# Optimization experiments

Hardware: AMD Instinct MI355X
Metric: run time of the kernel (lower is better)

The kernel has to match this reference:

```python
import jax, jax.numpy as jnp
import numpy as np

N_P, N_I, DIM = 30, 40, 6
W_I, C1, C2, LAM = 0.7, 1.5, 1.5, 0.3
EPS = 1e-8


def _decode(pos):
    # pos: [P, 6] -> per-particle fusion weights via pairwise softmax
    e = jnp.exp(pos[:, :4])
    fg_s = e[:, 0] + e[:, 1] + EPS
    bg_s = e[:, 2] + e[:, 3] + EPS
    return e[:, 0] / fg_s, e[:, 1] / fg_s, e[:, 2] / bg_s, e[:, 3] / bg_s


def _fitness(pos, rgb, dep, mask, r_dep):
    # rgb, dep, mask, r_dep: [H, W]; pos: [P, 6] -> scores [P]
    rgb_fg, dep_fg, rgb_bg, dep_bg = _decode(pos)
    mn = mask - mask.mean()
    mn_norm = jnp.linalg.norm(mn) + EPS
    fg = rgb_fg[:, None, None] * rgb + dep_fg[:, None, None] * dep   # [P,H,W]
    bg = rgb_bg[:, None, None] * rgb + dep_bg[:, None, None] * dep
    fused = mask * fg + (1.0 - mask) * bg
    fn = fused - fused.mean(axis=(1, 2), keepdims=True)
    fn_norm = jnp.sqrt((fn * fn).sum(axis=(1, 2)))
    ncc = (fn * mn).sum(axis=(1, 2)) / (fn_norm * mn_norm + EPS)
    pen_fg = ((1.0 - r_dep) * mask).mean()
    pen_bg = ((1.0 - r_dep) * (1.0 - mask)).mean()
    rel_pen = dep_fg * pen_fg + dep_bg * pen_bg
    return ncc - LAM * rel_pen


def _pso(rgb, dep, mask, r_dep):
    # Deterministic PSO with fixed RNG key; inputs are [H, W] maps.
    key = jax.random.key(42)
    k_pos, k_vel, k_r1, k_r2 = jax.random.split(key, 4)
    pos = jax.random.uniform(k_pos, (N_P, DIM), minval=-2.0, maxval=2.0)
    vel = jax.random.uniform(k_vel, (N_P, DIM), minval=-0.5, maxval=0.5)
    r1s = jax.random.uniform(k_r1, (N_I, N_P, DIM))
    r2s = jax.random.uniform(k_r2, (N_I, N_P, DIM))

    pb_pos = pos
    pb_fit = _fitness(pos, rgb, dep, mask, r_dep)
    gi = jnp.argmax(pb_fit)
    gb_pos = pb_pos[gi]
    gb_fit = pb_fit[gi]

    def step(carry, rs):
        pos, vel, pb_pos, pb_fit, gb_pos, gb_fit = carry
        r1, r2 = rs
        vel = W_I * vel + C1 * r1 * (pb_pos - pos) + C2 * r2 * (gb_pos - pos)
        pos = jnp.clip(pos + vel, -3.0, 3.0)
        fit = _fitness(pos, rgb, dep, mask, r_dep)
        better = fit > pb_fit
        pb_pos = jnp.where(better[:, None], pos, pb_pos)
        pb_fit = jnp.where(better, fit, pb_fit)
        bi = jnp.argmax(pb_fit)
        improve = pb_fit[bi] > gb_fit
        gb_pos = jnp.where(improve, pb_pos[bi], gb_pos)
        gb_fit = jnp.where(improve, pb_fit[bi], gb_fit)
        return (pos, vel, pb_pos, pb_fit, gb_pos, gb_fit), None

    (pos, vel, pb_pos, pb_fit, gb_pos, gb_fit), _ = jax.lax.scan(
        step, (pos, vel, pb_pos, pb_fit, gb_pos, gb_fit), (r1s, r2s))
    rgb_fg, dep_fg, rgb_bg, dep_bg = _decode(gb_pos[None, :])
    return rgb_fg[0], dep_fg[0], rgb_bg[0], dep_bg[0]


def _cos_sim(feat, proto):
    # feat [B,C,H,W], proto [B,C] -> [B,H,W]; matches F.normalize (clamp_min eps)
    p = proto / jnp.maximum(jnp.linalg.norm(proto, axis=1, keepdims=True), 1e-12)
    fnorm = jnp.maximum(jnp.sqrt((feat * feat).sum(axis=1, keepdims=True)), 1e-12)
    f = feat / fnorm
    return jnp.einsum('bchw,bc->bhw', f, p)


def setup_inputs() -> dict:
    key = jax.random.key(0)
    ks = jax.random.split(key, 10)
    B, C, H, W = 8, 256, 64, 64
    return {
        'f_rgb': jax.random.normal(ks[0], (B, C, H, W), dtype=jnp.float32),
        'f_depth': jax.random.normal(ks[1], (B, C, H, W), dtype=jnp.float32),
        'r_rgb': jax.random.uniform(ks[2], (B, 1, H, W), dtype=jnp.float32),
        'r_depth': jax.random.uniform(ks[3], (B, 1, H, W), dtype=jnp.float32),
        'proto_rgb': jax.random.normal(ks[4], (B, C), dtype=jnp.float32),
        'proto_dep': jax.random.normal(ks[5], (B, C), dtype=jnp.float32),
        'query_mask': jax.random.uniform(ks[6], (B, 1, H, W), dtype=jnp.float32),
        'conv_w': jax.random.normal(ks[7], (C, C), dtype=jnp.float32) * 0.05,
        'bn_gamma': jax.random.uniform(ks[8], (C,), dtype=jnp.float32),
        'bn_beta': jax.random.normal(ks[9], (C,), dtype=jnp.float32) * 0.1,
        'bn_mean': jnp.zeros((C,), dtype=jnp.float32),
        'bn_var': jnp.ones((C,), dtype=jnp.float32),
    }


def reference(f_rgb, f_depth, r_rgb, r_depth, proto_rgb, proto_dep, query_mask,
              conv_w, bn_gamma, bn_beta, bn_mean, bn_var):
    # cosine similarity maps [B,H,W]
    rgb_sim = _cos_sim(f_rgb, proto_rgb)
    dep_sim = _cos_sim(f_depth, proto_dep)

    # PSO operates on detached batch-mean maps (torch .detach().mean(0).cpu())
    sg = jax.lax.stop_gradient
    np_rgb = sg(rgb_sim).mean(axis=0)                 # [H,W]
    np_dep = sg(dep_sim).mean(axis=0)                 # [H,W]
    np_mask = sg(query_mask)[:, 0].mean(axis=0)       # mask already at (H,W): nearest interp is identity
    np_r_dep = sg(r_depth)[:, 0].mean(axis=0)
    rgb_fg, dep_fg, rgb_bg, dep_bg = _pso(np_rgb, np_dep, np_mask, np_r_dep)

    f_fg = rgb_fg * f_rgb + dep_fg * f_depth
    f_bg = rgb_bg * f_rgb + dep_bg * f_depth
    proxy = jax.nn.sigmoid((rgb_sim + dep_sim)[:, None] * 3.0)   # [B,1,H,W]
    f_fused = proxy * f_fg + (1.0 - proxy) * f_bg

    # post_proj: 1x1 conv (no bias) -> BN (eval) -> ReLU
    y = jnp.einsum('oc,bchw->bohw', conv_w, f_fused)
    inv = bn_gamma / jnp.sqrt(bn_var + 1e-5)
    y = y * inv[None, :, None, None] + (bn_beta - bn_mean * inv)[None, :, None, None]
    return jax.nn.relu(y)
```

## Files before the change

### kernel.cpp

```cpp
#include <hip/hip_runtime.h>
#include <stdint.h>
#include <float.h>

static constexpr size_t WS_SIM_RGB = 4096;
static constexpr size_t WS_SIM_DEP = 36864;
static constexpr size_t WS_NPMAPS  = 69632;
static constexpr size_t WS_STATS   = 86016;
static constexpr size_t WS_POUT    = 86048;
static constexpr size_t WS_RNG     = 90112;

typedef short short8 __attribute__((ext_vector_type(8)));
typedef float f32x4 __attribute__((ext_vector_type(4)));

__device__ __forceinline__ uint32_t pack_bf2(float a, float b) {
  uint32_t ua = __float_as_uint(a), ub = __float_as_uint(b);
  uint32_t ra = (ua + 0x7fffu + ((ua >> 16) & 1u)) >> 16;
  uint32_t rb = (ub + 0x7fffu + ((ub >> 16) & 1u)) >> 16;
  return (ra & 0xffffu) | (rb << 16);
}

__device__ __forceinline__ void threefry2x32(uint32_t k0, uint32_t k1,
                                             uint32_t c0, uint32_t c1,
                                             uint32_t& o0, uint32_t& o1) {
  uint32_t ks2 = k0 ^ k1 ^ 0x1BD11BDAu;
  uint32_t x0 = c0 + k0;
  uint32_t x1 = c1 + k1;
#define TF_ROUND(r) { x0 += x1; x1 = (x1 << (r)) | (x1 >> (32 - (r))); x1 ^= x0; }
  TF_ROUND(13) TF_ROUND(15) TF_ROUND(26) TF_ROUND(6)
  x0 += k1;  x1 += ks2 + 1u;
  TF_ROUND(17) TF_ROUND(29) TF_ROUND(16) TF_ROUND(24)
  x0 += ks2; x1 += k0 + 2u;
  TF_ROUND(13) TF_ROUND(15) TF_ROUND(26) TF_ROUND(6)
  x0 += k0;  x1 += k1 + 3u;
  TF_ROUND(17) TF_ROUND(29) TF_ROUND(16) TF_ROUND(24)
  x0 += k1;  x1 += ks2 + 4u;
  TF_ROUND(13) TF_ROUND(15) TF_ROUND(26) TF_ROUND(6)
  x0 += ks2; x1 += k0 + 5u;
#undef TF_ROUND
  o0 = x0; o1 = x1;
}

__device__ __forceinline__ float tf_u01(uint32_t k0, uint32_t k1, uint32_t idx) {
  uint32_t o0, o1;
  threefry2x32(k0, k1, 0u, idx, o0, o1);
  uint32_t bits = o0 ^ o1;
  uint32_t fb = (bits >> 9) | 0x3F800000u;
  return __uint_as_float(fb) - 1.0f;
}

__global__ __launch_bounds__(256) void sim_kernel(
    const float* __restrict__ f_rgb, const float* __restrict__ f_dep,
    const float* __restrict__ proto_rgb, const float* __restrict__ proto_dep,
    float* __restrict__ sim_rgb, float* __restrict__ sim_dep) {
  int tid = threadIdx.x;
  int bm = blockIdx.y;
  int b = bm >> 1, mo = bm & 1;
  const float* f  = mo ? f_dep : f_rgb;
  const float* pr = mo ? proto_dep : proto_rgb;
  float* sim = mo ? sim_dep : sim_rgb;
  __shared__ float shp[256];
  __shared__ float wsum[4];
  float pv = pr[b * 256 + tid];
  float ss0 = pv * pv;
#pragma unroll
  for (int off = 32; off > 0; off >>= 1) ss0 += __shfl_xor(ss0, off, 64);
  if ((tid & 63) == 0) wsum[tid >> 6] = ss0;
  __syncthreads();
  float nrm = fmaxf(sqrtf(wsum[0] + wsum[1] + wsum[2] + wsum[3]), 1e-12f);
  shp[tid] = pv / nrm;
  __syncthreads();
  int p = blockIdx.x * 256 + tid;
  const float* base = f + (size_t)b * 256 * 4096 + p;
  float dot = 0.f, ss = 0.f;
#pragma unroll 8
  for (int c = 0; c < 256; ++c) {
    float x = base[(size_t)c * 4096];
    dot += x * shp[c];
    ss  += x * x;
  }
  float fn = fmaxf(sqrtf(ss), 1e-12f);
  sim[b * 4096 + p] = dot / fn;
}

__global__ __launch_bounds__(256) void npmaps_kernel(
    const float* __restrict__ sim_rgb, const float* __restrict__ sim_dep,
    const float* __restrict__ qmask, const float* __restrict__ r_dep,
    float* __restrict__ npm) {
  int i = blockIdx.x * 256 + threadIdx.x;
  float sr = 0.f, sd = 0.f, sm = 0.f, sq = 0.f;
#pragma unroll
  for (int b = 0; b < 8; ++b) {
    sr += sim_rgb[b * 4096 + i];
    sd += sim_dep[b * 4096 + i];
    sm += qmask[b * 4096 + i];
    sq += r_dep[b * 4096 + i];
  }
  npm[i]          = sr * 0.125f;
  npm[4096 + i]   = sd * 0.125f;
  npm[8192 + i]   = sm * 0.125f;
  npm[12288 + i]  = sq * 0.125f;
}

__global__ __launch_bounds__(256) void stats_kernel(const float* __restrict__ npm,
                                                    float* __restrict__ stats) {
  const float* np_rgb  = npm;
  const float* np_dep  = npm + 4096;
  const float* np_mask = npm + 8192;
  const float* np_rdep = npm + 12288;
  __shared__ float col[17][257];
  __shared__ float res1[17];
  __shared__ float res2[5];
  int tid = threadIdx.x;
  float acc[17];
#pragma unroll
  for (int k = 0; k < 17; ++k) acc[k] = 0.f;
  for (int i = tid; i < 4096; i += 256) {
    float m = np_mask[i], r = np_rgb[i], d = np_dep[i], q = np_rdep[i];
    float om = 1.f - m;
    float M1 = m * r, M2 = m * d, M3 = om * r, M4 = om * d;
    acc[0] += m;
    acc[1] += M1; acc[2] += M2; acc[3] += M3; acc[4] += M4;
    acc[5] += M1 * M1; acc[6] += M1 * M2; acc[7] += M1 * M3; acc[8] += M1 * M4;
    acc[9] += M2 * M2; acc[10] += M2 * M3; acc[11] += M2 * M4;
    acc[12] += M3 * M3; acc[13] += M3 * M4; acc[14] += M4 * M4;
    float oq = 1.f - q;
    acc[15] += oq * m; acc[16] += oq * om;
  }
#pragma unroll
  for (int k = 0; k < 17; ++k) col[k][tid] = acc[k];
  __syncthreads();
  if (tid < 17) { float s = 0.f; for (int i = 0; i < 256; ++i) s += col[tid][i]; res1[tid] = s; }
  __syncthreads();
  float mask_mean = res1[0] * (1.f / 4096.f);
  float a2[5] = {0.f, 0.f, 0.f, 0.f, 0.f};
  for (int i = tid; i < 4096; i += 256) {
    float m = np_mask[i], r = np_rgb[i], d = np_dep[i];
    float om = 1.f - m;
    float mn = m - mask_mean;
    a2[0] += m * r * mn; a2[1] += m * d * mn;
    a2[2] += om * r * mn; a2[3] += om * d * mn;
    a2[4] += mn * mn;
  }
  __syncthreads();
#pragma unroll
  for (int k = 0; k < 5; ++k) col[k][tid] = a2[k];
  __syncthreads();
  if (tid < 5) { float s = 0.f; for (int i = 0; i < 256; ++i) s += col[tid][i]; res2[tid] = s; }
  __syncthreads();
  if (tid == 0) {
    stats[0] = res1[1]; stats[1] = res1[2]; stats[2] = res1[3]; stats[3] = res1[4];
    float G11 = res1[5], G12 = res1[6], G13 = res1[7], G14 = res1[8];
    float G22 = res1[9], G23 = res1[10], G24 = res1[11];
    float G33 = res1[12], G34 = res1[13], G44 = res1[14];
    float Gf[16] = {G11, G12, G13, G14,  G12, G22, G23, G24,
                    G13, G23, G33, G34,  G14, G24, G34, G44};
    for (int k = 0; k < 16; ++k) stats[4 + k] = Gf[k];
    stats[20] = res2[0]; stats[21] = res2[1]; stats[22] = res2[2]; stats[23] = res2[3];
    stats[24] = sqrtf(res2[4]) + 1e-8f;
    stats[25] = res1[15] * (1.f / 4096.f);
    stats[26] = res1[16] * (1.f / 4096.f);
  }
}

__global__ __launch_bounds__(256) void rng_kernel(float* __restrict__ rng) {
  int g = blockIdx.x * 256 + threadIdx.x;
  if (g >= 14760) return;
  int kind; uint32_t splitIdx, ctr, dst;
  if (g < 180) {
    kind = 0; splitIdx = 0; ctr = (uint32_t)g; dst = (uint32_t)g;
  } else if (g < 360) {
    kind = 1; splitIdx = 1; ctr = (uint32_t)(g - 180); dst = (uint32_t)g;
  } else if (g < 7560) {
    uint32_t c = (uint32_t)(g - 360);
    kind = 2; splitIdx = 2; ctr = c;
    uint32_t t = c / 180u, rem = c % 180u, p = rem / 6u, d = rem % 6u;
    dst = 360u + t * 360u + p * 12u + d;
  } else {
    uint32_t c = (uint32_t)(g - 7560);
    kind = 3; splitIdx = 3; ctr = c;
    uint32_t t = c / 180u, rem = c % 180u, p = rem / 6u, d = rem % 6u;
    dst = 360u + t * 360u + p * 12u + 6u + d;
  }
  uint32_t k0, k1;
  threefry2x32(0u, 42u, 0u, splitIdx, k0, k1);
  float u = tf_u01(k0, k1, ctr);
  float v;
  if (kind == 0)      v = fmaxf(-2.0f, u * 4.0f - 2.0f);
  else if (kind == 1) v = fmaxf(-0.5f, u - 0.5f);
  else                v = u;
  rng[dst] = v;
}

__device__ __forceinline__ float pso_fitness_fast(const float pos[6],
    const float S[4], const float G[16], const float V[4],
    float mn_norm, float pen_fg, float pen_bg) {
  float e0 = __expf(pos[0]), e1 = __expf(pos[1]);
  float e2 = __expf(pos[2]), e3 = __expf(pos[3]);
  float rf = __builtin_amdgcn_rcpf(e0 + e1 + 1e-8f);
  float rb = __builtin_amdgcn_rcpf(e2 + e3 + 1e-8f);
  float w[4] = {e0 * rf, e1 * rf, e2 * rb, e3 * rb};
  float num = 0.f, mus = 0.f;
#pragma unroll
  for (int k = 0; k < 4; ++k) { num += w[k] * V[k]; mus += w[k] * S[k]; }
  float q = 0.f;
#pragma unroll
  for (int j = 0; j < 4; ++j)
#pragma unroll
    for (int k = 0; k < 4; ++k) q += w[j] * G[j * 4 + k] * w[k];
  float fn2 = fmaxf(q - mus * mus * (1.f / 4096.f), 0.f);
  float den = __builtin_amdgcn_sqrtf(fn2) * mn_norm + 1e-8f;
  float ncc = num * __builtin_amdgcn_rcpf(den);
  return ncc - 0.3f * (w[1] * pen_fg + w[3] * pen_bg);
}

__device__ __forceinline__ float wavemax_lo32(float v) {
  int x = __float_as_int(v);
#define DPP_STEP(ctrl) { \
    int y = __builtin_amdgcn_update_dpp(x, x, ctrl, 0xf, 0xf, false); \
    x = __float_as_int(fmaxf(__int_as_float(x), __int_as_float(y))); }
  DPP_STEP(0x128)
  DPP_STEP(0x124)
  DPP_STEP(0x122)
  DPP_STEP(0x121)
#undef DPP_STEP
  float r0 = __int_as_float(__builtin_amdgcn_readlane(x, 0));
  float r1 = __int_as_float(__builtin_amdgcn_readlane(x, 16));
  return fmaxf(r0, r1);
}

__global__ void pso_kernel(const float* __restrict__ stats,
                           const float* __restrict__ rng,
                           float* __restrict__ pout) {
  int lane = threadIdx.x;
  bool act = lane < 30;
  float S[4], G[16], V[4];
#pragma unroll
  for (int k = 0; k < 4; ++k) S[k] = stats[k];
#pragma unroll
  for (int k = 0; k < 16; ++k) G[k] = stats[4 + k];
#pragma unroll
  for (int k = 0; k < 4; ++k) V[k] = stats[20 + k];
  float mn_norm = stats[24], pen_fg = stats[25], pen_bg = stats[26];

  float pos[6], vel[6], pbp[6];
#pragma unroll
  for (int d = 0; d < 6; ++d) { pos[d] = 0.f; vel[d] = 0.f; }
  if (act) {
#pragma unroll
    for (int d = 0; d < 6; ++d) {
      pos[d] = rng[lane * 6 + d];
      vel[d] = rng[180 + lane * 6 + d];
    }
  }
#pragma unroll
  for (int d = 0; d < 6; ++d) pbp[d] = pos[d];

  float f0 = pso_fitness_fast(pos, S, G, V, mn_norm, pen_fg, pen_bg);
  float pbf = act ? f0 : -FLT_MAX;

  float gbf = wavemax_lo32(pbf);
  float gb[6];
  {
    unsigned long long mm = __ballot(pbf == gbf);
    int bl = __ffsll(mm) - 1;
#pragma unroll
    for (int d = 0; d < 6; ++d)
      gb[d] = __int_as_float(__builtin_amdgcn_readlane(__float_as_int(pbp[d]), bl));
  }

  const float* rbase = rng + 360;
  float4 A0, A1, A2, B0, B1, B2;
  {
    const float4* p0 = (const float4*)(rbase + lane * 12);
    A0 = p0[0]; A1 = p0[1]; A2 = p0[2];
    const float4* p1 = (const float4*)(rbase + 360 + lane * 12);
    B0 = p1[0]; B1 = p1[1]; B2 = p1[2];
  }

#define PSO_ITER(R0, R1, R2, TNEXT) { \
    float r1v[6] = {R0.x, R0.y, R0.z, R0.w, R1.x, R1.y}; \
    float r2v[6] = {R1.z, R1.w, R2.x, R2.y, R2.z, R2.w}; \
    const float4* pf = (const float4*)(rbase + (TNEXT) * 360 + lane * 12); \
    R0 = pf[0]; R1 = pf[1]; R2 = pf[2]; \
    _Pragma("unroll") \
    for (int d = 0; d < 6; ++d) { \
      vel[d] = 0.7f * vel[d] + 1.5f * r1v[d] * (pbp[d] - pos[d]) \
                             + 1.5f * r2v[d] * (gb[d] - pos[d]); \
      pos[d] = fmaxf(-3.0f, fminf(pos[d] + vel[d], 3.0f)); \
    } \
    float f = pso_fitness_fast(pos, S, G, V, mn_norm, pen_fg, pen_bg); \
    if (act && f > pbf) { \
      pbf = f; \
      _Pragma("unroll") for (int d = 0; d < 6; ++d) pbp[d] = pos[d]; \
    } \
    float maxv = wavemax_lo32(pbf); \
    if (maxv > gbf) {     \
      unsigned long long mm = __ballot(pbf == maxv); \
      int bl = __ffsll(mm) - 1; \
      gbf = maxv; \
      _Pragma("unroll") for (int d = 0; d < 6; ++d) \
        gb[d] = __int_as_float(__builtin_amdgcn_readlane(__float_as_int(pbp[d]), bl)); \
    } \
  }

  for (int k = 0; k < 20; ++k) {
    PSO_ITER(A0, A1, A2, 2 * k + 2)
    PSO_ITER(B0, B1, B2, 2 * k + 3)
  }
#undef PSO_ITER

  if (lane == 0) {
    float e0 = expf(gb[0]), e1 = expf(gb[1]), e2 = expf(gb[2]), e3 = expf(gb[3]);
    float fgs = e0 + e1 + 1e-8f, bgs = e2 + e3 + 1e-8f;
    pout[0] = e0 / fgs;
    pout[1] = e1 / fgs;
    pout[2] = e2 / bgs;
    pout[3] = e3 / bgs;
  }
}

__global__ __launch_bounds__(512, 4) void gemm_kernel(
    const float* __restrict__ f_rgb, const float* __restrict__ f_dep,
    const float* __restrict__ sim_rgb, const float* __restrict__ sim_dep,
    const float* __restrict__ pout, const float* __restrict__ W,
    const float* __restrict__ bn_g, const float* __restrict__ bn_b,
    const float* __restrict__ bn_m, const float* __restrict__ bn_v,
    float* __restrict__ out) {
  __shared__ __align__(16) uint32_t As[2][128 * 20];
  __shared__ __align__(16) uint32_t Bs[2][128 * 17];
  const int tid = threadIdx.x;
  const int nt = blockIdx.x, mt = blockIdx.y, b = blockIdx.z;
  const int n0 = nt * 128, m0 = mt * 128;
  const size_t fbase = (size_t)b * 256 * 4096;

  const int bnn = tid & 127, bkq = tid >> 7;
  const int gi = b * 4096 + n0 + bnn;
  const float s = sim_rgb[gi] + sim_dep[gi];
  const float prb = 1.f / (1.f + expf(-3.f * s));
  const float pa = pout[0], pb = pout[1], pc = pout[2], pd = pout[3];
  const float abx = prb * pa + (1.f - prb) * pc;
  const float aby = prb * pb + (1.f - prb) * pd;
  const float* frb = f_rgb + fbase + n0 + bnn;
  const float* fdb = f_dep + fbase + n0 + bnn;
  const int ak2 = tid & 15, amr = tid >> 4;
  const int lane = tid & 63, wv = tid >> 6;
  const int wm = wv >> 2, wn = wv & 3;
  const int lg = lane >> 4, ln = lane & 15;

  f32x4 acc[4][2];
#pragma unroll
  for (int i = 0; i < 4; ++i)
#pragma unroll
    for (int j = 0; j < 2; ++j) acc[i][j] = (f32x4)0.f;

  float pr0[4], pr1[4], pd0[4], pd1[4];
  float2 pw[4];

#define LOAD_STEP(S) { \
    const int k0_ = (S) * 32; \
    _Pragma("unroll") \
    for (int q = 0; q < 4; ++q) { \
      size_t ko = (size_t)(k0_ + 2 * (bkq * 4 + q)) * 4096; \
      pr0[q] = frb[ko]; pr1[q] = frb[ko + 4096]; \
      pd0[q] = fdb[ko]; pd1[q] = fdb[ko + 4096]; \
    } \
    _Pragma("unroll") \
    for (int p = 0; p < 4; ++p) \
      pw[p] = *(const float2*)(W + (size_t)(m0 + amr + p * 32) * 256 + k0_ + 2 * ak2); \
  }

#define PACK_WRITE(BUF) { \
    _Pragma("unroll") \
    for (int q = 0; q < 4; ++q) \
      Bs[BUF][bnn * 17 + bkq * 4 + q] = \
          pack_bf2(abx * pr0[q] + aby * pd0[q], abx * pr1[q] + aby * pd1[q]); \
    _Pragma("unroll") \
    for (int p = 0; p < 4; ++p) \
      As[BUF][(amr + p * 32) * 20 + ak2] = pack_bf2(pw[p].x, pw[p].y); \
  }

  LOAD_STEP(0)
  PACK_WRITE(0)
  __syncthreads();

  for (int s8 = 0; s8 < 8; ++s8) {
    const int cur = s8 & 1;
    if (s8 < 7) LOAD_STEP(s8 + 1)
    short8 af[4], bf[2];
#pragma unroll
    for (int i = 0; i < 4; ++i) {
      int m = wm * 64 + i * 16 + ln;
      float4 t = *(const float4*)(&As[cur][m * 20 + lg * 4]);
      af[i] = *(short8*)&t;
    }
#pragma unroll
    for (int j = 0; j < 2; ++j) {
      int n = wn * 32 + j * 16 + ln;
      const uint32_t* bp = &Bs[cur][n * 17 + lg * 4];
      union { uint32_t w[4]; short8 v; } u;
      u.w[0] = bp[0]; u.w[1] = bp[1]; u.w[2] = bp[2]; u.w[3] = bp[3];
      bf[j] = u.v;
    }
#pragma unroll
    for (int i = 0; i < 4; ++i)
#pragma unroll
      for (int j = 0; j < 2; ++j)
        acc[i][j] = __builtin_amdgcn_mfma_f32_16x16x32_bf16(af[i], bf[j], acc[i][j], 0, 0, 0);
    if (s8 < 7) PACK_WRITE(cur ^ 1)
    __syncthreads();
  }
#undef LOAD_STEP
#undef PACK_WRITE

#pragma unroll
  for (int i = 0; i < 4; ++i) {
#pragma unroll
    for (int r = 0; r < 4; ++r) {
      int m = m0 + wm * 64 + i * 16 + lg * 4 + r;
      float inv = bn_g[m] / sqrtf(bn_v[m] + 1e-5f);
      float sh = bn_b[m] - bn_m[m] * inv;
      float* orow = out + ((size_t)(b * 256 + m)) * 4096 + n0 + wn * 32 + ln;
#pragma unroll
      for (int j = 0; j < 2; ++j)
        orow[j * 16] = fmaxf(acc[i][j][r] * inv + sh, 0.f);
    }
  }
}

extern "C" void kernel_launch(void* const* d_in, const int* in_sizes, int n_in,
                              void* d_out, int out_size, void* d_ws, size_t ws_size,
                              hipStream_t stream) {
  (void)in_sizes; (void)n_in; (void)out_size; (void)ws_size;
  const float* f_rgb     = (const float*)d_in[0];
  const float* f_depth   = (const float*)d_in[1];
  const float* r_depth   = (const float*)d_in[3];
  const float* proto_rgb = (const float*)d_in[4];
  const float* proto_dep = (const float*)d_in[5];
  const float* qmask     = (const float*)d_in[6];
  const float* conv_w    = (const float*)d_in[7];
  const float* bn_g      = (const float*)d_in[8];
  const float* bn_b      = (const float*)d_in[9];
  const float* bn_m      = (const float*)d_in[10];
  const float* bn_v      = (const float*)d_in[11];
  float* out = (float*)d_out;
  float* ws  = (float*)d_ws;

  float* sim_rgb = ws + WS_SIM_RGB;
  float* sim_dep = ws + WS_SIM_DEP;
  float* npm     = ws + WS_NPMAPS;
  float* stats   = ws + WS_STATS;
  float* pout    = ws + WS_POUT;
  float* rng     = ws + WS_RNG;

  rng_kernel<<<dim3(58), dim3(256), 0, stream>>>(rng);
  sim_kernel<<<dim3(16, 16), dim3(256), 0, stream>>>(f_rgb, f_depth, proto_rgb,
                                                     proto_dep, sim_rgb, sim_dep);
  npmaps_kernel<<<dim3(16), dim3(256), 0, stream>>>(sim_rgb, sim_dep, qmask, r_depth, npm);
  stats_kernel<<<dim3(1), dim3(256), 0, stream>>>(npm, stats);
  pso_kernel<<<dim3(1), dim3(64), 0, stream>>>(stats, rng, pout);
  gemm_kernel<<<dim3(32, 2, 8), dim3(512), 0, stream>>>(f_rgb, f_depth, sim_rgb, sim_dep,
                                                        pout, conv_w,
                                                        bn_g, bn_b, bn_m, bn_v, out);
}
```

Baseline: 78.96 us.

## Fuse stats into PSO kernel and vectorize GEMM global loads

After: 80.29 us. Within noise of the previous version (+1.7%).

```diff
diff --git a/kernel.cpp b/kernel.cpp
--- a/kernel.cpp
+++ b/kernel.cpp
@@ -5,7 +5,6 @@
 static constexpr size_t WS_SIM_RGB = 4096;
 static constexpr size_t WS_SIM_DEP = 36864;
 static constexpr size_t WS_NPMAPS  = 69632;
-static constexpr size_t WS_STATS   = 86016;
 static constexpr size_t WS_POUT    = 86048;
 static constexpr size_t WS_RNG     = 90112;
 
@@ -101,67 +100,6 @@
   npm[12288 + i]  = sq * 0.125f;
 }
 
-__global__ __launch_bounds__(256) void stats_kernel(const float* __restrict__ npm,
-                                                    float* __restrict__ stats) {
-  const float* np_rgb  = npm;
-  const float* np_dep  = npm + 4096;
-  const float* np_mask = npm + 8192;
-  const float* np_rdep = npm + 12288;
-  __shared__ float col[17][257];
-  __shared__ float res1[17];
-  __shared__ float res2[5];
-  int tid = threadIdx.x;
-  float acc[17];
-#pragma unroll
-  for (int k = 0; k < 17; ++k) acc[k] = 0.f;
-  for (int i = tid; i < 4096; i += 256) {
-    float m = np_mask[i], r = np_rgb[i], d = np_dep[i], q = np_rdep[i];
-    float om = 1.f - m;
-    float M1 = m * r, M2 = m * d, M3 = om * r, M4 = om * d;
-    acc[0] += m;
-    acc[1] += M1; acc[2] += M2; acc[3] += M3; acc[4] += M4;
-    acc[5] += M1 * M1; acc[6] += M1 * M2; acc[7] += M1 * M3; acc[8] += M1 * M4;
-    acc[9] += M2 * M2; acc[10] += M2 * M3; acc[11] += M2 * M4;
-    acc[12] += M3 * M3; acc[13] += M3 * M4; acc[14] += M4 * M4;
-    float oq = 1.f - q;
-    acc[15] += oq * m; acc[16] += oq * om;
-  }
-#pragma unroll
-  for (int k = 0; k < 17; ++k) col[k][tid] = acc[k];
-  __syncthreads();
-  if (tid < 17) { float s = 0.f; for (int i = 0; i < 256; ++i) s += col[tid][i]; res1[tid] = s; }
-  __syncthreads();
-  float mask_mean = res1[0] * (1.f / 4096.f);
-  float a2[5] = {0.f, 0.f, 0.f, 0.f, 0.f};
-  for (int i = tid; i < 4096; i += 256) {
-    float m = np_mask[i], r = np_rgb[i], d = np_dep[i];
-    float om = 1.f - m;
-    float mn = m - mask_mean;
-    a2[0] += m * r * mn; a2[1] += m * d * mn;
-    a2[2] += om * r * mn; a2[3] += om * d * mn;
-    a2[4] += mn * mn;
-  }
-  __syncthreads();
-#pragma unroll
-  for (int k = 0; k < 5; ++k) col[k][tid] = a2[k];
-  __syncthreads();
-  if (tid < 5) { float s = 0.f; for (int i = 0; i < 256; ++i) s += col[tid][i]; res2[tid] = s; }
-  __syncthreads();
-  if (tid == 0) {
-    stats[0] = res1[1]; stats[1] = res1[2]; stats[2] = res1[3]; stats[3] = res1[4];
-    float G11 = res1[5], G12 = res1[6], G13 = res1[7], G14 = res1[8];
-    float G22 = res1[9], G23 = res1[10], G24 = res1[11];
-    float G33 = res1[12], G34 = res1[13], G44 = res1[14];
-    float Gf[16] = {G11, G12, G13, G14,  G12, G22, G23, G24,
-                    G13, G23, G33, G34,  G14, G24, G34, G44};
-    for (int k = 0; k < 16; ++k) stats[4 + k] = Gf[k];
-    stats[20] = res2[0]; stats[21] = res2[1]; stats[22] = res2[2]; stats[23] = res2[3];
-    stats[24] = sqrtf(res2[4]) + 1e-8f;
-    stats[25] = res1[15] * (1.f / 4096.f);
-    stats[26] = res1[16] * (1.f / 4096.f);
-  }
-}
-
 __global__ __launch_bounds__(256) void rng_kernel(float* __restrict__ rng) {
   int g = blockIdx.x * 256 + threadIdx.x;
   if (g >= 14760) return;
@@ -228,19 +166,81 @@
   return fmaxf(r0, r1);
 }
 
-__global__ void pso_kernel(const float* __restrict__ stats,
-                           const float* __restrict__ rng,
-                           float* __restrict__ pout) {
-  int lane = threadIdx.x;
+__global__ __launch_bounds__(256) void stats_pso_kernel(
+    const float* __restrict__ npm, const float* __restrict__ rng,
+    float* __restrict__ pout) {
+  const float* np_rgb  = npm;
+  const float* np_dep  = npm + 4096;
+  const float* np_mask = npm + 8192;
+  const float* np_rdep = npm + 12288;
+  __shared__ float col[17][257];
+  __shared__ float res1[17];
+  __shared__ float res2[5];
+  __shared__ float sst[27];
+  int tid = threadIdx.x;
+  {
+    float acc[17];
+#pragma unroll
+    for (int k = 0; k < 17; ++k) acc[k] = 0.f;
+    for (int i = tid; i < 4096; i += 256) {
+      float m = np_mask[i], r = np_rgb[i], d = np_dep[i], q = np_rdep[i];
+      float om = 1.f - m;
+      float M1 = m * r, M2 = m * d, M3 = om * r, M4 = om * d;
+      acc[0] += m;
+      acc[1] += M1; acc[2] += M2; acc[3] += M3; acc[4] += M4;
+      acc[5] += M1 * M1; acc[6] += M1 * M2; acc[7] += M1 * M3; acc[8] += M1 * M4;
+      acc[9] += M2 * M2; acc[10] += M2 * M3; acc[11] += M2 * M4;
+      acc[12] += M3 * M3; acc[13] += M3 * M4; acc[14] += M4 * M4;
+      float oq = 1.f - q;
+      acc[15] += oq * m; acc[16] += oq * om;
+    }
+#pragma unroll
+    for (int k = 0; k < 17; ++k) col[k][tid] = acc[k];
+    __syncthreads();
+    if (tid < 17) { float s = 0.f; for (int i = 0; i < 256; ++i) s += col[tid][i]; res1[tid] = s; }
+    __syncthreads();
+    float mask_mean = res1[0] * (1.f / 4096.f);
+    float a2[5] = {0.f, 0.f, 0.f, 0.f, 0.f};
+    for (int i = tid; i < 4096; i += 256) {
+      float m = np_mask[i], r = np_rgb[i], d = np_dep[i];
+      float om = 1.f - m;
+      float mn = m - mask_mean;
+      a2[0] += m * r * mn; a2[1] += m * d * mn;
+      a2[2] += om * r * mn; a2[3] += om * d * mn;
+      a2[4] += mn * mn;
+    }
+    __syncthreads();
+#pragma unroll
+    for (int k = 0; k < 5; ++k) col[k][tid] = a2[k];
+    __syncthreads();
+    if (tid < 5) { float s = 0.f; for (int i = 0; i < 256; ++i) s += col[tid][i]; res2[tid] = s; }
+    __syncthreads();
+    if (tid == 0) {
+      sst[0] = res1[1]; sst[1] = res1[2]; sst[2] = res1[3]; sst[3] = res1[4];
+      float G11 = res1[5], G12 = res1[6], G13 = res1[7], G14 = res1[8];
+      float G22 = res1[9], G23 = res1[10], G24 = res1[11];
+      float G33 = res1[12], G34 = res1[13], G44 = res1[14];
+      float Gf[16] = {G11, G12, G13, G14,  G12, G22, G23, G24,
+                      G13, G23, G33, G34,  G14, G24, G34, G44};
+      for (int k = 0; k < 16; ++k) sst[4 + k] = Gf[k];
+      sst[20] = res2[0]; sst[21] = res2[1]; sst[22] = res2[2]; sst[23] = res2[3];
+      sst[24] = sqrtf(res2[4]) + 1e-8f;
+      sst[25] = res1[15] * (1.f / 4096.f);
+      sst[26] = res1[16] * (1.f / 4096.f);
+    }
+    __syncthreads();
+  }
+  if (tid >= 64) return;
+  int lane = tid;
   bool act = lane < 30;
   float S[4], G[16], V[4];
 #pragma unroll
-  for (int k = 0; k < 4; ++k) S[k] = stats[k];
-#pragma unroll
-  for (int k = 0; k < 16; ++k) G[k] = stats[4 + k];
-#pragma unroll
-  for (int k = 0; k < 4; ++k) V[k] = stats[20 + k];
-  float mn_norm = stats[24], pen_fg = stats[25], pen_bg = stats[26];
+  for (int k = 0; k < 4; ++k) S[k] = sst[k];
+#pragma unroll
+  for (int k = 0; k < 16; ++k) G[k] = sst[4 + k];
+#pragma unroll
+  for (int k = 0; k < 4; ++k) V[k] = sst[20 + k];
+  float mn_norm = sst[24], pen_fg = sst[25], pen_bg = sst[26];
 
   float pos[6], vel[6], pbp[6];
 #pragma unroll
@@ -333,16 +333,26 @@
   const int n0 = nt * 128, m0 = mt * 128;
   const size_t fbase = (size_t)b * 256 * 4096;
 
-  const int bnn = tid & 127, bkq = tid >> 7;
-  const int gi = b * 4096 + n0 + bnn;
-  const float s = sim_rgb[gi] + sim_dep[gi];
-  const float prb = 1.f / (1.f + expf(-3.f * s));
+  const int p0 = (tid & 31) * 4;
+  const int bkp = tid >> 5;
   const float pa = pout[0], pb = pout[1], pc = pout[2], pd = pout[3];
-  const float abx = prb * pa + (1.f - prb) * pc;
-  const float aby = prb * pb + (1.f - prb) * pd;
-  const float* frb = f_rgb + fbase + n0 + bnn;
-  const float* fdb = f_dep + fbase + n0 + bnn;
-  const int ak2 = tid & 15, amr = tid >> 4;
+  float abx[4], aby[4];
+  {
+    const int gi = b * 4096 + n0 + p0;
+    const f32x4 sr = *(const f32x4*)(sim_rgb + gi);
+    const f32x4 sd = *(const f32x4*)(sim_dep + gi);
+#pragma unroll
+    for (int i = 0; i < 4; ++i) {
+      float s = sr[i] + sd[i];
+      float prb = 1.f / (1.f + expf(-3.f * s));
+      abx[i] = prb * pa + (1.f - prb) * pc;
+      aby[i] = prb * pb + (1.f - prb) * pd;
+    }
+  }
+  const float* frb = f_rgb + fbase + n0 + p0;
+  const float* fdb = f_dep + fbase + n0 + p0;
+  const int am = tid & 127, akq = tid >> 7;
+  const float* wrow = W + (size_t)(m0 + am) * 256 + akq * 8;
   const int lane = tid & 63, wv = tid >> 6;
   const int wm = wv >> 2, wn = wv & 3;
   const int lg = lane >> 4, ln = lane & 15;
@@ -353,30 +363,29 @@
 #pragma unroll
     for (int j = 0; j < 2; ++j) acc[i][j] = (f32x4)0.f;
 
-  float pr0[4], pr1[4], pd0[4], pd1[4];
-  float2 pw[4];
+  f32x4 vr0, vr1, vd0, vd1, vw0, vw1;
 
 #define LOAD_STEP(S) { \
-    const int k0_ = (S) * 32; \
-    _Pragma("unroll") \
-    for (int q = 0; q < 4; ++q) { \
-      size_t ko = (size_t)(k0_ + 2 * (bkq * 4 + q)) * 4096; \
-      pr0[q] = frb[ko]; pr1[q] = frb[ko + 4096]; \
-      pd0[q] = fdb[ko]; pd1[q] = fdb[ko + 4096]; \
-    } \
-    _Pragma("unroll") \
-    for (int p = 0; p < 4; ++p) \
-      pw[p] = *(const float2*)(W + (size_t)(m0 + amr + p * 32) * 256 + k0_ + 2 * ak2); \
+    const size_t ko = (size_t)((S) * 32 + 2 * bkp) * 4096; \
+    vr0 = *(const f32x4*)(frb + ko); \
+    vr1 = *(const f32x4*)(frb + ko + 4096); \
+    vd0 = *(const f32x4*)(fdb + ko); \
+    vd1 = *(const f32x4*)(fdb + ko + 4096); \
+    vw0 = *(const f32x4*)(wrow + (S) * 32); \
+    vw1 = *(const f32x4*)(wrow + (S) * 32 + 4); \
   }
 
 #define PACK_WRITE(BUF) { \
     _Pragma("unroll") \
-    for (int q = 0; q < 4; ++q) \
-      Bs[BUF][bnn * 17 + bkq * 4 + q] = \
-          pack_bf2(abx * pr0[q] + aby * pd0[q], abx * pr1[q] + aby * pd1[q]); \
-    _Pragma("unroll") \
-    for (int p = 0; p < 4; ++p) \
-      As[BUF][(amr + p * 32) * 20 + ak2] = pack_bf2(pw[p].x, pw[p].y); \
+    for (int i = 0; i < 4; ++i) \
+      Bs[BUF][(p0 + i) * 17 + bkp] = \
+          pack_bf2(abx[i] * vr0[i] + aby[i] * vd0[i], abx[i] * vr1[i] + aby[i] * vd1[i]); \
+    uint32_t aw0 = pack_bf2(vw0[0], vw0[1]); \
+    uint32_t aw1 = pack_bf2(vw0[2], vw0[3]); \
+    uint32_t aw2 = pack_bf2(vw1[0], vw1[1]); \
+    uint32_t aw3 = pack_bf2(vw1[2], vw1[3]); \
+    uint32_t* ap = &As[BUF][am * 20 + akq * 4]; \
+    ap[0] = aw0; ap[1] = aw1; ap[2] = aw2; ap[3] = aw3; \
   }
 
   LOAD_STEP(0)
@@ -448,7 +457,6 @@
   float* sim_rgb = ws + WS_SIM_RGB;
   float* sim_dep = ws + WS_SIM_DEP;
   float* npm     = ws + WS_NPMAPS;
-  float* stats   = ws + WS_STATS;
   float* pout    = ws + WS_POUT;
   float* rng     = ws + WS_RNG;
 
@@ -456,8 +464,7 @@
   sim_kernel<<<dim3(16, 16), dim3(256), 0, stream>>>(f_rgb, f_depth, proto_rgb,
                                                      proto_dep, sim_rgb, sim_dep);
   npmaps_kernel<<<dim3(16), dim3(256), 0, stream>>>(sim_rgb, sim_dep, qmask, r_depth, npm);
-  stats_kernel<<<dim3(1), dim3(256), 0, stream>>>(npm, stats);
-  pso_kernel<<<dim3(1), dim3(64), 0, stream>>>(stats, rng, pout);
+  stats_pso_kernel<<<dim3(1), dim3(256), 0, stream>>>(npm, rng, pout);
   gemm_kernel<<<dim3(32, 2, 8), dim3(512), 0, stream>>>(f_rgb, f_depth, sim_rgb, sim_dep,
                                                         pout, conv_w,
                                                         bn_g, bn_b, bn_m, bn_v, out);
```
